# Optimization experiments

Measured on AMD Instinct MI355X. Metric: run time of the kernel, lower is better.

The kernel has to match this reference:

```python
import jax, jax.numpy as jnp
import numpy as np

N_NODES = 50000
N_EDGES = 800000
FEAT_IN = 128
POS_IN = 16
EDGE_FEAT_IN = 16
H = 64
L = 4


def _lin(k, fan_in, fan_out):
    kw, kb = jax.random.split(k)
    s = 1.0 / np.sqrt(fan_in)
    W = jax.random.uniform(kw, (fan_in, fan_out), minval=-s, maxval=s, dtype=jnp.float32)
    b = jax.random.uniform(kb, (fan_out,), minval=-s, maxval=s, dtype=jnp.float32)
    return W, b


def setup_inputs() -> dict:
    key = jax.random.key(0)
    ks = jax.random.split(key, 32)
    h = jax.random.normal(ks[0], (N_NODES, FEAT_IN), dtype=jnp.float32)
    e = jax.random.normal(ks[1], (N_EDGES, EDGE_FEAT_IN), dtype=jnp.float32)
    p = jax.random.normal(ks[2], (N_NODES, POS_IN), dtype=jnp.float32)
    edge_index = jax.random.randint(ks[3], (2, N_EDGES), 0, N_NODES, dtype=jnp.int64 if jax.config.x64_enabled else jnp.int32)
    he_W, he_b = _lin(ks[4], FEAT_IN, H)
    ee_W, ee_b = _lin(ks[5], EDGE_FEAT_IN, H)
    pe_W, pe_b = _lin(ks[6], POS_IN, H)

    def stack(fan_in, base):
        Ws, bs = [], []
        for i in range(L):
            W, b = _lin(jax.random.fold_in(ks[7], base * 100 + i), fan_in, H)
            Ws.append(W); bs.append(b)
        return jnp.stack(Ws), jnp.stack(bs)

    hm_W, hm_b = stack(5 * H, 0)  # h_message_mlp
    hu_W, hu_b = stack(2 * H, 1)  # h_update
    eu_W, eu_b = stack(3 * H, 2)  # e_update
    pm_W, pm_b = stack(3 * H, 3)  # p_message_mlp
    pu_W, pu_b = stack(2 * H, 4)  # p_update
    return dict(h=h, e=e, p=p, edge_index=edge_index,
                he_W=he_W, he_b=he_b, ee_W=ee_W, ee_b=ee_b, pe_W=pe_W, pe_b=pe_b,
                hm_W=hm_W, hm_b=hm_b, hu_W=hu_W, hu_b=hu_b,
                eu_W=eu_W, eu_b=eu_b, pm_W=pm_W, pm_b=pm_b, pu_W=pu_W, pu_b=pu_b)


def reference(h, e, p, edge_index, he_W, he_b, ee_W, ee_b, pe_W, pe_b,
              hm_W, hm_b, hu_W, hu_b, eu_W, eu_b, pm_W, pm_b, pu_W, pu_b):
    send, rec = edge_index[0], edge_index[1]
    n = h.shape[0]
    h = h @ he_W + he_b  # [N,H]
    e = e @ ee_W + ee_b  # [E,H]
    p = p @ pe_W + pe_b  # [N,H]
    for i in range(L):
        hp_send = jnp.concatenate((h[send], p[send]), axis=1)  # [E,2H]
        hp_rec = jnp.concatenate((h[rec], p[rec]), axis=1)     # [E,2H]
        h_msg = jnp.concatenate((hp_send, hp_rec, e), axis=1) @ hm_W[i] + hm_b[i]  # [E,H]
        h_agg = jax.ops.segment_sum(h_msg, rec, num_segments=n)  # [N,H]
        h = jnp.concatenate((h, h_agg), axis=1) @ hu_W[i] + hu_b[i]
        e = jnp.concatenate((h[send], h[rec], e), axis=1) @ eu_W[i] + eu_b[i]
        p_msg = jnp.concatenate((p[send], p[rec], e), axis=1) @ pm_W[i] + pm_b[i]
        p_agg = jax.ops.segment_sum(p_msg, rec, num_segments=n)
        p = jnp.concatenate((p, p_agg), axis=1) @ pu_W[i] + pu_b[i]
    return (h, p)
```

## Files before the change

kernel.cpp:

```cpp
#include <hip/hip_runtime.h>
#include <hip/hip_bf16.h>

#define NN 50000
#define NE 800000

typedef __hip_bfloat16 bf16;
typedef __attribute__((ext_vector_type(8))) short bf16x8s;
typedef __attribute__((ext_vector_type(4))) float f32x4;

#define OFF_HP     0L
#define OFF_HSUM   12800000L
#define OFF_PSUM   25600000L
#define OFF_ESUM   38400000L
#define OFF_EAGGA  41600000L
#define OFF_EAGGB  54400000L
#define OFF_WFMT   67200000L
#define OFF_ROWPTR 67716096L
#define OFF_COLIDX 67916100L
#define OFF_SSEND  71116100L
#define OFF_SEG    74316100L
#define OFF_CNT    77516100L
#define OFF_BSUM   77716100L

#define SCAN_B 196

#define FW_HE 0
#define FW_EE 8192
#define FW_PE 10240
#define FW_L0 12288
#define LSTR  61440
#define R_HAGG 0
#define R_HMR  12288
#define R_HU   20480
#define R_EUS  28672
#define R_EUR  32768
#define R_EUE  36864
#define R_PAGG 40960
#define R_PMR  49152
#define R_PU   53248

#define AGG_STRIDE 72

__device__ __forceinline__ bf16x8s bfrag(const bf16* w, int c, int t, int lane) {
    return *(const bf16x8s*)(w + ((long)(c*4 + t)*64 + lane)*8);
}
__device__ __forceinline__ bf16x8s cvt8(const float* fp) {
    float4 f0 = ((const float4*)fp)[0];
    float4 f1 = ((const float4*)fp)[1];
    bf16 tmp[8];
    tmp[0]=__float2bfloat16(f0.x); tmp[1]=__float2bfloat16(f0.y);
    tmp[2]=__float2bfloat16(f0.z); tmp[3]=__float2bfloat16(f0.w);
    tmp[4]=__float2bfloat16(f1.x); tmp[5]=__float2bfloat16(f1.y);
    tmp[6]=__float2bfloat16(f1.z); tmp[7]=__float2bfloat16(f1.w);
    return *(const bf16x8s*)tmp;
}

__global__ __launch_bounds__(256) void wfmt_k(
    const float* __restrict__ he, const float* __restrict__ ee, const float* __restrict__ pe,
    const float* __restrict__ hm, const float* __restrict__ hu, const float* __restrict__ eu,
    const float* __restrict__ pm, const float* __restrict__ pu, bf16* __restrict__ wf)
{
    int s = blockIdx.x;
    const float* src = nullptr; int rowoff = 0, Ksrc = 0, Kpad = 0, mode = 0, split = 0, gap = 0; long doff = 0;
    if      (s == 0) { src = he; Ksrc = 128; Kpad = 128; doff = FW_HE; }
    else if (s == 1) { src = ee; Ksrc = 16;  Kpad = 32;  doff = FW_EE; }
    else if (s == 2) { src = pe; Ksrc = 16;  Kpad = 32;  doff = FW_PE; }
    else {
        int i = (s - 3) / 9, g = (s - 3) % 9;
        long base = FW_L0 + (long)i*LSTR;
        const float* HM = hm + (long)i*320*64;
        const float* HU = hu + (long)i*128*64;
        const float* EU = eu + (long)i*192*64;
        const float* PM = pm + (long)i*192*64;
        const float* PU = pu + (long)i*128*64;
        switch (g) {
          case 0:  src=HM; mode=4; split=128; gap=128; Kpad=192; doff=base+R_HAGG; break;
          case 1:  src=HM; rowoff=128; Ksrc=128; Kpad=128; doff=base+R_HMR;  break;
          case 2:  src=HU; rowoff=0;   Ksrc=128; Kpad=128; doff=base+R_HU;   break;
          case 3:  src=EU; rowoff=0;   Ksrc=64;  Kpad=64;  doff=base+R_EUS;  break;
          case 4:  src=EU; rowoff=64;  Ksrc=64;  Kpad=64;  doff=base+R_EUR;  break;
          case 5:  src=EU; rowoff=128; Ksrc=64;  Kpad=64;  doff=base+R_EUE;  break;
          case 6:  src=PM; mode=4; split=64; gap=64; Kpad=128; doff=base+R_PAGG; break;
          case 7:  src=PM; rowoff=64;  Ksrc=64;  Kpad=64;  doff=base+R_PMR;  break;
          default: src=PU; rowoff=0;   Ksrc=128; Kpad=128; doff=base+R_PU;   break;
        }
    }
    int total = Kpad * 64;
    for (int idx = threadIdx.x; idx < total; idx += 256) {
        int j = idx & 7, l = (idx >> 3) & 63, ct = idx >> 9;
        int c = ct >> 2, t = ct & 3;
        int k = c*32 + (l >> 4)*8 + j;
        int n = t*16 + (l & 15);
        float v;
        if (mode == 4) v = src[(long)(k + (k >= split ? gap : 0))*64 + n];
        else           v = (k < Ksrc) ? src[(long)(rowoff + k)*64 + n] : 0.f;
        wf[doff + idx] = __float2bfloat16(v);
    }
}

__global__ __launch_bounds__(256) void hist_k(const int* __restrict__ rec, int* __restrict__ cnt)
{
    int e = blockIdx.x*256 + threadIdx.x;
    if (e < NE) atomicAdd(&cnt[rec[e]], 1);
}

__global__ __launch_bounds__(256) void scan1_k(const int* __restrict__ cnt, int* __restrict__ bsum)
{
    __shared__ int sdata[256];
    int tid = threadIdx.x;
    int i = blockIdx.x*256 + tid;
    sdata[tid] = (i < NN) ? cnt[i] : 0;
    __syncthreads();
    #pragma unroll
    for (int off = 128; off > 0; off >>= 1) {
        if (tid < off) sdata[tid] += sdata[tid + off];
        __syncthreads();
    }
    if (tid == 0) bsum[blockIdx.x] = sdata[0];
}

__global__ __launch_bounds__(256) void scan2_k(int* __restrict__ bsum)
{
    __shared__ int sdata[256];
    int tid = threadIdx.x;
    int v = (tid < SCAN_B) ? bsum[tid] : 0;
    sdata[tid] = v;
    __syncthreads();
    #pragma unroll
    for (int off = 1; off < 256; off <<= 1) {
        int t = (tid >= off) ? sdata[tid - off] : 0;
        __syncthreads();
        sdata[tid] += t;
        __syncthreads();
    }
    if (tid < SCAN_B) bsum[tid] = sdata[tid] - v;
}

__global__ __launch_bounds__(256) void scan3_k(const int* __restrict__ cnt,
    const int* __restrict__ bsum, int* __restrict__ rowptr)
{
    __shared__ int sdata[256];
    int tid = threadIdx.x;
    int i = blockIdx.x*256 + tid;
    sdata[tid] = (i < NN) ? cnt[i] : 0;
    __syncthreads();
    #pragma unroll
    for (int off = 1; off < 256; off <<= 1) {
        int t = (tid >= off) ? sdata[tid - off] : 0;
        __syncthreads();
        sdata[tid] += t;
        __syncthreads();
    }
    if (i < NN) rowptr[i + 1] = sdata[tid] + bsum[blockIdx.x];
    if (i == 0) rowptr[0] = 0;
}

__global__ __launch_bounds__(256) void scatter_k(const int* __restrict__ rec,
    const int* __restrict__ rowptr, int* __restrict__ cursor, int* __restrict__ colidx)
{
    int e = blockIdx.x*256 + threadIdx.x;
    if (e < NE) {
        int r = rec[e];
        int pos = atomicAdd(&cursor[r], 1);
        colidx[rowptr[r] + pos] = e;
    }
}

__global__ __launch_bounds__(256) void segfill_k(const int* __restrict__ rowptr, int* __restrict__ seg)
{
    int n = blockIdx.x*256 + threadIdx.x;
    if (n < NN) {
        int b = rowptr[n], e = rowptr[n + 1];
        for (int j = b; j < e; ++j) seg[j] = n;
    }
}

template <bool BOTH>
__global__ __launch_bounds__(256) void gsum64_k(const bf16* __restrict__ hp, int coff,
    const int* __restrict__ ssend, const int* __restrict__ seg,
    float* __restrict__ out1, float* __restrict__ out2)
{
    __shared__ int s_ids[256];
    __shared__ int s_seg[256];
    int tid = threadIdx.x, lane = tid & 63, wv = tid >> 6;
    int gbase = blockIdx.x*256;
    s_ids[tid] = ssend[gbase + tid];
    s_seg[tid] = seg[gbase + tid];
    __syncthreads();
    int j0 = wv*64;
    const bf16* base = hp + coff + lane;

    unsigned short va[16], vb[16], wa[16], wb[16];
    #pragma unroll
    for (int k = 0; k < 16; ++k) {
        long o = (long)s_ids[j0 + k]*128;
        va[k] = *(const unsigned short*)(base + o);
        if (BOTH) wa[k] = *(const unsigned short*)(base + o + 64);
    }

    float a = 0.f, b2 = 0.f;
    int cur = s_seg[j0];
    #pragma unroll
    for (int b = 0; b < 4; ++b) {
        if (b < 3) {
            #pragma unroll
            for (int k = 0; k < 16; ++k) {
                long o = (long)s_ids[j0 + (b+1)*16 + k]*128;
                vb[k] = *(const unsigned short*)(base + o);
                if (BOTH) wb[k] = *(const unsigned short*)(base + o + 64);
            }
        }
        #pragma unroll
        for (int k = 0; k < 16; ++k) {
            int n = s_seg[j0 + b*16 + k];
            if (n != cur) {
                atomicAdd(&out1[(long)cur*64 + lane], a);
                if (BOTH) atomicAdd(&out2[(long)cur*64 + lane], b2);
                a = 0.f; b2 = 0.f; cur = n;
            }
            a += __uint_as_float(((unsigned)va[k]) << 16);
            if (BOTH) b2 += __uint_as_float(((unsigned)wa[k]) << 16);
        }
        if (b < 3) {
            #pragma unroll
            for (int k = 0; k < 16; ++k) { va[k] = vb[k]; if (BOTH) wa[k] = wb[k]; }
        }
    }
    atomicAdd(&out1[(long)cur*64 + lane], a);
    if (BOTH) atomicAdd(&out2[(long)cur*64 + lane], b2);
}

__global__ __launch_bounds__(256) void esum_k(const float* __restrict__ e_in,
    const int* __restrict__ colidx, const int* __restrict__ seg, const int* __restrict__ send,
    int* __restrict__ ssend, float* __restrict__ esum)
{
    __shared__ int s_ids[256];
    __shared__ int s_seg[256];
    int tid = threadIdx.x;
    int gbase = blockIdx.x*256;
    int id = colidx[gbase + tid];
    s_ids[tid] = id;
    s_seg[tid] = seg[gbase + tid];
    ssend[gbase + tid] = send[id];
    __syncthreads();
    int grp = tid >> 4, c = tid & 15;
    int j0 = grp*16;
    float vv[16];
    #pragma unroll
    for (int jj = 0; jj < 16; ++jj) vv[jj] = e_in[(long)s_ids[j0 + jj]*16 + c];
    float a = 0.f;
    int cur = s_seg[j0];
    #pragma unroll
    for (int jj = 0; jj < 16; ++jj) {
        int n = s_seg[j0 + jj];
        if (n != cur) { atomicAdd(&esum[(long)cur*16 + c], a); a = 0.f; cur = n; }
        a += vv[jj];
    }
    atomicAdd(&esum[(long)cur*16 + c], a);
}

__global__ __launch_bounds__(256) void eembn_k(const float* __restrict__ esum,
    const int* __restrict__ deg, const bf16* __restrict__ wEE, const float* __restrict__ ee_b,
    float* __restrict__ eagg)
{
    int tid = threadIdx.x, lane = tid & 63, wv = tid >> 6;
    int l15 = lane & 15, q = lane >> 4;
    int row = blockIdx.x*64 + wv*16 + l15;
    int rc = (row < NN) ? row : NN - 1;
    f32x4 acc[4];
    #pragma unroll
    for (int t = 0; t < 4; ++t) { acc[t][0]=0; acc[t][1]=0; acc[t][2]=0; acc[t][3]=0; }
    {
        bf16x8s af = {0,0,0,0,0,0,0,0};
        if (q < 2) af = cvt8(esum + (long)rc*16 + q*8);
        #pragma unroll
        for (int t = 0; t < 4; ++t)
            acc[t] = __builtin_amdgcn_mfma_f32_16x16x32_bf16(af, bfrag(wEE, 0, t, lane), acc[t], 0, 0, 0);
    }
    float bv[4];
    #pragma unroll
    for (int t = 0; t < 4; ++t) bv[t] = ee_b[t*16 + l15];
    #pragma unroll
    for (int r = 0; r < 4; ++r) {
        int ro = blockIdx.x*64 + wv*16 + q*4 + r;
        if (ro < NN) {
            float dg = (float)deg[ro];
            #pragma unroll
            for (int t = 0; t < 4; ++t)
                eagg[(long)ro*64 + t*16 + l15] = acc[t][r] + dg*bv[t];
        }
    }
}

__global__ __launch_bounds__(256) void hemb_k(const float* __restrict__ h_in,
    const bf16* __restrict__ wHE, const float* __restrict__ he_b, bf16* __restrict__ hp)
{
    int tid = threadIdx.x, lane = tid & 63, wv = tid >> 6;
    int l15 = lane & 15, q = lane >> 4;
    int row = blockIdx.x*64 + wv*16 + l15;
    int rc = (row < NN) ? row : NN - 1;
    f32x4 acc[4];
    #pragma unroll
    for (int t = 0; t < 4; ++t) { float b = he_b[t*16 + l15]; acc[t][0]=b; acc[t][1]=b; acc[t][2]=b; acc[t][3]=b; }
    #pragma unroll
    for (int c = 0; c < 4; ++c) {
        bf16x8s af = cvt8(h_in + (long)rc*128 + c*32 + q*8);
        #pragma unroll
        for (int t = 0; t < 4; ++t)
            acc[t] = __builtin_amdgcn_mfma_f32_16x16x32_bf16(af, bfrag(wHE, c, t, lane), acc[t], 0, 0, 0);
    }
    #pragma unroll
    for (int r = 0; r < 4; ++r) {
        int ro = blockIdx.x*64 + wv*16 + q*4 + r;
        if (ro < NN)
            #pragma unroll
            for (int t = 0; t < 4; ++t) hp[(long)ro*128 + t*16 + l15] = __float2bfloat16(acc[t][r]);
    }
}

__global__ __launch_bounds__(256) void pemb_k(const float* __restrict__ p_in,
    const bf16* __restrict__ wPE, const float* __restrict__ pe_b, bf16* __restrict__ hp)
{
    int tid = threadIdx.x, lane = tid & 63, wv = tid >> 6;
    int l15 = lane & 15, q = lane >> 4;
    int row = blockIdx.x*64 + wv*16 + l15;
    int rc = (row < NN) ? row : NN - 1;
    f32x4 acc[4];
    #pragma unroll
    for (int t = 0; t < 4; ++t) { float b = pe_b[t*16 + l15]; acc[t][0]=b; acc[t][1]=b; acc[t][2]=b; acc[t][3]=b; }
    {
        bf16x8s af = {0,0,0,0,0,0,0,0};
        if (q < 2) af = cvt8(p_in + (long)rc*16 + q*8);
        #pragma unroll
        for (int t = 0; t < 4; ++t)
            acc[t] = __builtin_amdgcn_mfma_f32_16x16x32_bf16(af, bfrag(wPE, 0, t, lane), acc[t], 0, 0, 0);
    }
    #pragma unroll
    for (int r = 0; r < 4; ++r) {
        int ro = blockIdx.x*64 + wv*16 + q*4 + r;
        if (ro < NN)
            #pragma unroll
            for (int t = 0; t < 4; ++t) hp[(long)ro*128 + 64 + t*16 + l15] = __float2bfloat16(acc[t][r]);
    }
}

__global__ __launch_bounds__(256) void hfuse_k(
    bf16* __restrict__ hp, float* __restrict__ hsum, const float* __restrict__ psum,
    const float* __restrict__ eagg, const int* __restrict__ deg,
    const bf16* __restrict__ wAGG, const bf16* __restrict__ wR, const float* __restrict__ mb,
    const bf16* __restrict__ wU, const float* __restrict__ ub, float* __restrict__ out2)
{
    __shared__ __align__(16) bf16 sAgg[64 * AGG_STRIDE];
    int tid = threadIdx.x, lane = tid & 63, wv = tid >> 6;
    int l15 = lane & 15, q = lane >> 4;
    int row = blockIdx.x*64 + wv*16 + l15;
    int rc = (row < NN) ? row : NN - 1;

    f32x4 aA[4], aR[4];
    #pragma unroll
    for (int t = 0; t < 4; ++t) {
        aA[t][0]=0;aA[t][1]=0;aA[t][2]=0;aA[t][3]=0;
        aR[t][0]=0;aR[t][1]=0;aR[t][2]=0;aR[t][3]=0;
    }
    #pragma unroll
    for (int c = 0; c < 6; ++c) {
        bf16x8s af = (c < 2) ? cvt8(hsum + (long)rc*64 + c*32 + q*8)
                   : (c < 4) ? cvt8(psum + (long)rc*64 + (c-2)*32 + q*8)
                             : cvt8(eagg + (long)rc*64 + (c-4)*32 + q*8);
        #pragma unroll
        for (int t = 0; t < 4; ++t)
            aA[t] = __builtin_amdgcn_mfma_f32_16x16x32_bf16(af, bfrag(wAGG, c, t, lane), aA[t], 0, 0, 0);
    }
    if (row < NN) {
        float4 z4 = make_float4(0.f, 0.f, 0.f, 0.f);
        #pragma unroll
        for (int c = 0; c < 2; ++c) {
            *(float4*)(hsum + (long)rc*64 + c*32 + q*8)     = z4;
            *(float4*)(hsum + (long)rc*64 + c*32 + q*8 + 4) = z4;
        }
    }
    #pragma unroll
    for (int c = 0; c < 4; ++c) {
        bf16x8s af = *(const bf16x8s*)(hp + (long)rc*128 + c*32 + q*8);
        #pragma unroll
        for (int t = 0; t < 4; ++t)
            aR[t] = __builtin_amdgcn_mfma_f32_16x16x32_bf16(af, bfrag(wR, c, t, lane), aR[t], 0, 0, 0);
    }
    float mbv[4];
    #pragma unroll
    for (int t = 0; t < 4; ++t) mbv[t] = mb[t*16 + l15];
    #pragma unroll
    for (int r = 0; r < 4; ++r) {
        int ro = blockIdx.x*64 + wv*16 + q*4 + r;
        float dg = (float)deg[(ro < NN) ? ro : NN - 1];
        #pragma unroll
        for (int t = 0; t < 4; ++t)
            sAgg[(wv*16 + q*4 + r)*AGG_STRIDE + t*16 + l15] =
                __float2bfloat16(aA[t][r] + dg*(aR[t][r] + mbv[t]));
    }
    __syncthreads();
    f32x4 acc[4];
    #pragma unroll
    for (int t = 0; t < 4; ++t) { float b = ub[t*16 + l15]; acc[t][0]=b; acc[t][1]=b; acc[t][2]=b; acc[t][3]=b; }
    #pragma unroll
    for (int c = 0; c < 4; ++c) {
        bf16x8s af = (c < 2) ? *(const bf16x8s*)(hp + (long)rc*128 + c*32 + q*8)
                             : *(const bf16x8s*)(sAgg + (wv*16 + l15)*AGG_STRIDE + (c-2)*32 + q*8);
        #pragma unroll
        for (int t = 0; t < 4; ++t)
            acc[t] = __builtin_amdgcn_mfma_f32_16x16x32_bf16(af, bfrag(wU, c, t, lane), acc[t], 0, 0, 0);
    }
    #pragma unroll
    for (int r = 0; r < 4; ++r) {
        int ro = blockIdx.x*64 + wv*16 + q*4 + r;
        if (ro < NN) {
            #pragma unroll
            for (int t = 0; t < 4; ++t) {
                float fv = acc[t][r];
                hp[(long)ro*128 + t*16 + l15] = __float2bfloat16(fv);
                if (out2) out2[(long)ro*64 + t*16 + l15] = fv;
            }
        }
    }
}

__global__ __launch_bounds__(256) void pfuse_k(
    bf16* __restrict__ hp, const float* __restrict__ hsumN, float* __restrict__ psum,
    const float* __restrict__ eaggIn, float* __restrict__ eaggOut, const int* __restrict__ deg,
    const bf16* __restrict__ wEUS, const bf16* __restrict__ wEUR, const bf16* __restrict__ wEUE,
    const float* __restrict__ eub,
    const bf16* __restrict__ wAGG, const bf16* __restrict__ wR, const float* __restrict__ mb,
    const bf16* __restrict__ wU, const float* __restrict__ ub, float* __restrict__ out2)
{
    __shared__ __align__(16) bf16 sE[64 * AGG_STRIDE];
    __shared__ __align__(16) bf16 sAgg[64 * AGG_STRIDE];
    int tid = threadIdx.x, lane = tid & 63, wv = tid >> 6;
    int l15 = lane & 15, q = lane >> 4;
    int row = blockIdx.x*64 + wv*16 + l15;
    int rc = (row < NN) ? row : NN - 1;

    f32x4 aE[4], aH[4];
    #pragma unroll
    for (int t = 0; t < 4; ++t) {
        aE[t][0]=0;aE[t][1]=0;aE[t][2]=0;aE[t][3]=0;
        aH[t][0]=0;aH[t][1]=0;aH[t][2]=0;aH[t][3]=0;
    }
    #pragma unroll
    for (int c = 0; c < 4; ++c) {
        bf16x8s af = (c < 2) ? cvt8(hsumN + (long)rc*64 + c*32 + q*8)
                             : cvt8(eaggIn + (long)rc*64 + (c-2)*32 + q*8);
        #pragma unroll
        for (int t = 0; t < 4; ++t) {
            bf16x8s w = (c < 2) ? bfrag(wEUS, c, t, lane) : bfrag(wEUE, c-2, t, lane);
            aE[t] = __builtin_amdgcn_mfma_f32_16x16x32_bf16(af, w, aE[t], 0, 0, 0);
        }
    }
    #pragma unroll
    for (int c = 0; c < 2; ++c) {
        bf16x8s af = *(const bf16x8s*)(hp + (long)rc*128 + c*32 + q*8);
        #pragma unroll
        for (int t = 0; t < 4; ++t)
            aH[t] = __builtin_amdgcn_mfma_f32_16x16x32_bf16(af, bfrag(wEUR, c, t, lane), aH[t], 0, 0, 0);
    }
    float ebv[4];
    #pragma unroll
    for (int t = 0; t < 4; ++t) ebv[t] = eub[t*16 + l15];
    #pragma unroll
    for (int r = 0; r < 4; ++r) {
        int ro = blockIdx.x*64 + wv*16 + q*4 + r;
        float dg = (float)deg[(ro < NN) ? ro : NN - 1];
        #pragma unroll
        for (int t = 0; t < 4; ++t) {
            float ev = aE[t][r] + dg*(aH[t][r] + ebv[t]);
            sE[(wv*16 + q*4 + r)*AGG_STRIDE + t*16 + l15] = __float2bfloat16(ev);
            if (eaggOut && ro < NN) eaggOut[(long)ro*64 + t*16 + l15] = ev;
        }
    }
    __syncthreads();

    f32x4 aA[4], aR[4];
    #pragma unroll
    for (int t = 0; t < 4; ++t) {
        aA[t][0]=0;aA[t][1]=0;aA[t][2]=0;aA[t][3]=0;
        aR[t][0]=0;aR[t][1]=0;aR[t][2]=0;aR[t][3]=0;
    }
    #pragma unroll
    for (int c = 0; c < 4; ++c) {
        bf16x8s af = (c < 2) ? cvt8(psum + (long)rc*64 + c*32 + q*8)
                             : *(const bf16x8s*)(sE + (wv*16 + l15)*AGG_STRIDE + (c-2)*32 + q*8);
        #pragma unroll
        for (int t = 0; t < 4; ++t)
            aA[t] = __builtin_amdgcn_mfma_f32_16x16x32_bf16(af, bfrag(wAGG, c, t, lane), aA[t], 0, 0, 0);
    }
    if (row < NN) {
        float4 z4 = make_float4(0.f, 0.f, 0.f, 0.f);
        #pragma unroll
        for (int c = 0; c < 2; ++c) {
            *(float4*)(psum + (long)rc*64 + c*32 + q*8)     = z4;
            *(float4*)(psum + (long)rc*64 + c*32 + q*8 + 4) = z4;
        }
    }
    #pragma unroll
    for (int c = 0; c < 2; ++c) {
        bf16x8s af = *(const bf16x8s*)(hp + (long)rc*128 + 64 + c*32 + q*8);
        #pragma unroll
        for (int t = 0; t < 4; ++t)
            aR[t] = __builtin_amdgcn_mfma_f32_16x16x32_bf16(af, bfrag(wR, c, t, lane), aR[t], 0, 0, 0);
    }
    float mbv[4];
    #pragma unroll
    for (int t = 0; t < 4; ++t) mbv[t] = mb[t*16 + l15];
    #pragma unroll
    for (int r = 0; r < 4; ++r) {
        int ro = blockIdx.x*64 + wv*16 + q*4 + r;
        float dg = (float)deg[(ro < NN) ? ro : NN - 1];
        #pragma unroll
        for (int t = 0; t < 4; ++t)
            sAgg[(wv*16 + q*4 + r)*AGG_STRIDE + t*16 + l15] =
                __float2bfloat16(aA[t][r] + dg*(aR[t][r] + mbv[t]));
    }
    __syncthreads();
    f32x4 acc[4];
    #pragma unroll
    for (int t = 0; t < 4; ++t) { float b = ub[t*16 + l15]; acc[t][0]=b; acc[t][1]=b; acc[t][2]=b; acc[t][3]=b; }
    #pragma unroll
    for (int c = 0; c < 4; ++c) {
        bf16x8s af = (c < 2) ? *(const bf16x8s*)(hp + (long)rc*128 + 64 + c*32 + q*8)
                             : *(const bf16x8s*)(sAgg + (wv*16 + l15)*AGG_STRIDE + (c-2)*32 + q*8);
        #pragma unroll
        for (int t = 0; t < 4; ++t)
            acc[t] = __builtin_amdgcn_mfma_f32_16x16x32_bf16(af, bfrag(wU, c, t, lane), acc[t], 0, 0, 0);
    }
    #pragma unroll
    for (int r = 0; r < 4; ++r) {
        int ro = blockIdx.x*64 + wv*16 + q*4 + r;
        if (ro < NN) {
            #pragma unroll
            for (int t = 0; t < 4; ++t) {
                float fv = acc[t][r];
                hp[(long)ro*128 + 64 + t*16 + l15] = __float2bfloat16(fv);
                if (out2) out2[(long)ro*64 + t*16 + l15] = fv;
            }
        }
    }
}

extern "C" void kernel_launch(void* const* d_in, const int* in_sizes, int n_in,
                              void* d_out, int out_size, void* d_ws, size_t ws_size,
                              hipStream_t stream)
{
    (void)in_sizes; (void)n_in; (void)out_size; (void)ws_size;
    const float* h_in = (const float*)d_in[0];
    const float* e_in = (const float*)d_in[1];
    const float* p_in = (const float*)d_in[2];
    const int*  ei   = (const int*)d_in[3];
    const int* send = ei;
    const int* rec  = ei + NE;
    const float* he_W = (const float*)d_in[4];  const float* he_b = (const float*)d_in[5];
    const float* ee_W = (const float*)d_in[6];  const float* ee_b = (const float*)d_in[7];
    const float* pe_W = (const float*)d_in[8];  const float* pe_b = (const float*)d_in[9];
    const float* hm_W = (const float*)d_in[10]; const float* hm_b = (const float*)d_in[11];
    const float* hu_W = (const float*)d_in[12]; const float* hu_b = (const float*)d_in[13];
    const float* eu_W = (const float*)d_in[14]; const float* eu_b = (const float*)d_in[15];
    const float* pm_W = (const float*)d_in[16]; const float* pm_b = (const float*)d_in[17];
    const float* pu_W = (const float*)d_in[18]; const float* pu_b = (const float*)d_in[19];

    char* ws = (char*)d_ws;
    bf16* hp     = (bf16*)(ws + OFF_HP);
    float* hsum  = (float*)(ws + OFF_HSUM);
    float* psum  = (float*)(ws + OFF_PSUM);
    float* esum  = (float*)(ws + OFF_ESUM);
    float* eaggA = (float*)(ws + OFF_EAGGA);
    float* eaggB = (float*)(ws + OFF_EAGGB);
    bf16* wf     = (bf16*)(ws + OFF_WFMT);
    int* rowptr  = (int*)(ws + OFF_ROWPTR);
    int* colidx  = (int*)(ws + OFF_COLIDX);
    int* ssend   = (int*)(ws + OFF_SSEND);
    int* segarr  = (int*)(ws + OFF_SEG);
    int* cnt     = (int*)(ws + OFF_CNT);
    int* bsum    = (int*)(ws + OFF_BSUM);
    float* dout  = (float*)d_out;

    const int EB   = NE / 256;
    const int NB64 = (NN + 63) / 64;

    (void)hipMemsetAsync(cnt, 0, NN * sizeof(int), stream);
    hist_k<<<EB, 256, 0, stream>>>(rec, cnt);
    scan1_k<<<SCAN_B, 256, 0, stream>>>(cnt, bsum);
    scan2_k<<<1, 256, 0, stream>>>(bsum);
    scan3_k<<<SCAN_B, 256, 0, stream>>>(cnt, bsum, rowptr);
    (void)hipMemsetAsync(cnt, 0, NN * sizeof(int), stream);
    scatter_k<<<EB, 256, 0, stream>>>(rec, rowptr, cnt, colidx);
    segfill_k<<<SCAN_B, 256, 0, stream>>>(rowptr, segarr);

    (void)hipMemsetAsync(hsum, 0, (long)NN*(64 + 64 + 16)*sizeof(float), stream);

    esum_k<<<EB, 256, 0, stream>>>(e_in, colidx, segarr, send, ssend, esum);

    wfmt_k<<<39, 256, 0, stream>>>(he_W, ee_W, pe_W, hm_W, hu_W, eu_W, pm_W, pu_W, wf);

    hemb_k<<<NB64, 256, 0, stream>>>(h_in, wf + FW_HE, he_b, hp);
    pemb_k<<<NB64, 256, 0, stream>>>(p_in, wf + FW_PE, pe_b, hp);
    eembn_k<<<NB64, 256, 0, stream>>>(esum, cnt, wf + FW_EE, ee_b, eaggA);
    gsum64_k<true><<<EB, 256, 0, stream>>>(hp, 0, ssend, segarr, hsum, psum);

    float* eA = eaggA;
    float* eB = eaggB;
    for (int i = 0; i < 4; ++i) {
        long base = FW_L0 + (long)i*LSTR;
        hfuse_k<<<NB64, 256, 0, stream>>>(hp, hsum, psum, eA, cnt,
            wf + base + R_HAGG, wf + base + R_HMR, hm_b + i*64,
            wf + base + R_HU, hu_b + i*64,
            (i == 3) ? dout : nullptr);
        gsum64_k<false><<<EB, 256, 0, stream>>>(hp, 0, ssend, segarr, hsum, nullptr);
        pfuse_k<<<NB64, 256, 0, stream>>>(hp, hsum, psum, eA, (i < 3) ? eB : nullptr, cnt,
            wf + base + R_EUS, wf + base + R_EUR, wf + base + R_EUE, eu_b + i*64,
            wf + base + R_PAGG, wf + base + R_PMR, pm_b + i*64,
            wf + base + R_PU, pu_b + i*64,
            (i == 3) ? dout + (long)NN*64 : nullptr);
        if (i < 3)
            gsum64_k<false><<<EB, 256, 0, stream>>>(hp, 64, ssend, segarr, psum, nullptr);
        float* tmp = eA; eA = eB; eB = tmp;
    }
}
```

Baseline: 646.4 us.

## Store edge aggregates in bf16, fuse h/p embeddings, deepen gather prefetch

The per-node edge aggregate buffers change from fp32 to bf16, which halves their write and read traffic in eembn, hfuse and pfuse. The h and p embedding kernels become one launch that writes both halves of the hp row. The gather-sum kernel takes the prefetch depth as a template parameter and uses 32 loads in flight for the single-stream passes, trading extra registers for more memory-level parallelism. Keeping the edge aggregate in bf16 adds a rounding step that lowers its precision.

After: 657.3 us. About the same (+1.7%).

```diff
diff --git a/kernel.cpp b/kernel.cpp
--- a/kernel.cpp
+++ b/kernel.cpp
@@ -175,7 +175,7 @@
     }
 }
 
-template <bool BOTH>
+template <int DEPTH, bool BOTH>
 __global__ __launch_bounds__(256) void gsum64_k(const bf16* __restrict__ hp, int coff,
     const int* __restrict__ ssend, const int* __restrict__ seg,
     float* __restrict__ out1, float* __restrict__ out2)
@@ -189,10 +189,12 @@
     __syncthreads();
     int j0 = wv*64;
     const bf16* base = hp + coff + lane;
-
-    unsigned short va[16], vb[16], wa[16], wb[16];
-    #pragma unroll
-    for (int k = 0; k < 16; ++k) {
+    constexpr int NB = 64 / DEPTH;
+
+    unsigned short va[DEPTH], vb[DEPTH];
+    unsigned short wa[BOTH ? DEPTH : 1], wb[BOTH ? DEPTH : 1];
+    #pragma unroll
+    for (int k = 0; k < DEPTH; ++k) {
         long o = (long)s_ids[j0 + k]*128;
         va[k] = *(const unsigned short*)(base + o);
         if (BOTH) wa[k] = *(const unsigned short*)(base + o + 64);
@@ -201,18 +203,18 @@
     float a = 0.f, b2 = 0.f;
     int cur = s_seg[j0];
     #pragma unroll
-    for (int b = 0; b < 4; ++b) {
-        if (b < 3) {
+    for (int b = 0; b < NB; ++b) {
+        if (b < NB - 1) {
             #pragma unroll
-            for (int k = 0; k < 16; ++k) {
-                long o = (long)s_ids[j0 + (b+1)*16 + k]*128;
+            for (int k = 0; k < DEPTH; ++k) {
+                long o = (long)s_ids[j0 + (b+1)*DEPTH + k]*128;
                 vb[k] = *(const unsigned short*)(base + o);
                 if (BOTH) wb[k] = *(const unsigned short*)(base + o + 64);
             }
         }
         #pragma unroll
-        for (int k = 0; k < 16; ++k) {
-            int n = s_seg[j0 + b*16 + k];
+        for (int k = 0; k < DEPTH; ++k) {
+            int n = s_seg[j0 + b*DEPTH + k];
             if (n != cur) {
                 atomicAdd(&out1[(long)cur*64 + lane], a);
                 if (BOTH) atomicAdd(&out2[(long)cur*64 + lane], b2);
@@ -221,9 +223,9 @@
             a += __uint_as_float(((unsigned)va[k]) << 16);
             if (BOTH) b2 += __uint_as_float(((unsigned)wa[k]) << 16);
         }
-        if (b < 3) {
+        if (b < NB - 1) {
             #pragma unroll
-            for (int k = 0; k < 16; ++k) { va[k] = vb[k]; if (BOTH) wa[k] = wb[k]; }
+            for (int k = 0; k < DEPTH; ++k) { va[k] = vb[k]; if (BOTH) wa[k] = wb[k]; }
         }
     }
     atomicAdd(&out1[(long)cur*64 + lane], a);
@@ -261,7 +263,7 @@
 
 __global__ __launch_bounds__(256) void eembn_k(const float* __restrict__ esum,
     const int* __restrict__ deg, const bf16* __restrict__ wEE, const float* __restrict__ ee_b,
-    float* __restrict__ eagg)
+    bf16* __restrict__ eagg)
 {
     int tid = threadIdx.x, lane = tid & 63, wv = tid >> 6;
     int l15 = lane & 15, q = lane >> 4;
@@ -287,66 +289,56 @@
             float dg = (float)deg[ro];
             #pragma unroll
             for (int t = 0; t < 4; ++t)
-                eagg[(long)ro*64 + t*16 + l15] = acc[t][r] + dg*bv[t];
-        }
-    }
-}
-
-__global__ __launch_bounds__(256) void hemb_k(const float* __restrict__ h_in,
-    const bf16* __restrict__ wHE, const float* __restrict__ he_b, bf16* __restrict__ hp)
+                eagg[(long)ro*64 + t*16 + l15] = __float2bfloat16(acc[t][r] + dg*bv[t]);
+        }
+    }
+}
+
+__global__ __launch_bounds__(256) void hpemb_k(const float* __restrict__ h_in,
+    const float* __restrict__ p_in,
+    const bf16* __restrict__ wHE, const bf16* __restrict__ wPE,
+    const float* __restrict__ he_b, const float* __restrict__ pe_b, bf16* __restrict__ hp)
 {
     int tid = threadIdx.x, lane = tid & 63, wv = tid >> 6;
     int l15 = lane & 15, q = lane >> 4;
     int row = blockIdx.x*64 + wv*16 + l15;
     int rc = (row < NN) ? row : NN - 1;
-    f32x4 acc[4];
-    #pragma unroll
-    for (int t = 0; t < 4; ++t) { float b = he_b[t*16 + l15]; acc[t][0]=b; acc[t][1]=b; acc[t][2]=b; acc[t][3]=b; }
+    f32x4 aH[4], aP[4];
+    #pragma unroll
+    for (int t = 0; t < 4; ++t) {
+        float bh = he_b[t*16 + l15], bp = pe_b[t*16 + l15];
+        aH[t][0]=bh; aH[t][1]=bh; aH[t][2]=bh; aH[t][3]=bh;
+        aP[t][0]=bp; aP[t][1]=bp; aP[t][2]=bp; aP[t][3]=bp;
+    }
     #pragma unroll
     for (int c = 0; c < 4; ++c) {
         bf16x8s af = cvt8(h_in + (long)rc*128 + c*32 + q*8);
         #pragma unroll
         for (int t = 0; t < 4; ++t)
-            acc[t] = __builtin_amdgcn_mfma_f32_16x16x32_bf16(af, bfrag(wHE, c, t, lane), acc[t], 0, 0, 0);
+            aH[t] = __builtin_amdgcn_mfma_f32_16x16x32_bf16(af, bfrag(wHE, c, t, lane), aH[t], 0, 0, 0);
+    }
+    {
+        bf16x8s af = {0,0,0,0,0,0,0,0};
+        if (q < 2) af = cvt8(p_in + (long)rc*16 + q*8);
+        #pragma unroll
+        for (int t = 0; t < 4; ++t)
+            aP[t] = __builtin_amdgcn_mfma_f32_16x16x32_bf16(af, bfrag(wPE, 0, t, lane), aP[t], 0, 0, 0);
     }
     #pragma unroll
     for (int r = 0; r < 4; ++r) {
         int ro = blockIdx.x*64 + wv*16 + q*4 + r;
         if (ro < NN)
             #pragma unroll
-            for (int t = 0; t < 4; ++t) hp[(long)ro*128 + t*16 + l15] = __float2bfloat16(acc[t][r]);
-    }
-}
-
-__global__ __launch_bounds__(256) void pemb_k(const float* __restrict__ p_in,
-    const bf16* __restrict__ wPE, const float* __restrict__ pe_b, bf16* __restrict__ hp)
-{
-    int tid = threadIdx.x, lane = tid & 63, wv = tid >> 6;
-    int l15 = lane & 15, q = lane >> 4;
-    int row = blockIdx.x*64 + wv*16 + l15;
-    int rc = (row < NN) ? row : NN - 1;
-    f32x4 acc[4];
-    #pragma unroll
-    for (int t = 0; t < 4; ++t) { float b = pe_b[t*16 + l15]; acc[t][0]=b; acc[t][1]=b; acc[t][2]=b; acc[t][3]=b; }
-    {
-        bf16x8s af = {0,0,0,0,0,0,0,0};
-        if (q < 2) af = cvt8(p_in + (long)rc*16 + q*8);
-        #pragma unroll
-        for (int t = 0; t < 4; ++t)
-            acc[t] = __builtin_amdgcn_mfma_f32_16x16x32_bf16(af, bfrag(wPE, 0, t, lane), acc[t], 0, 0, 0);
-    }
-    #pragma unroll
-    for (int r = 0; r < 4; ++r) {
-        int ro = blockIdx.x*64 + wv*16 + q*4 + r;
-        if (ro < NN)
-            #pragma unroll
-            for (int t = 0; t < 4; ++t) hp[(long)ro*128 + 64 + t*16 + l15] = __float2bfloat16(acc[t][r]);
+            for (int t = 0; t < 4; ++t) {
+                hp[(long)ro*128 + t*16 + l15]      = __float2bfloat16(aH[t][r]);
+                hp[(long)ro*128 + 64 + t*16 + l15] = __float2bfloat16(aP[t][r]);
+            }
     }
 }
 
 __global__ __launch_bounds__(256) void hfuse_k(
     bf16* __restrict__ hp, float* __restrict__ hsum, const float* __restrict__ psum,
-    const float* __restrict__ eagg, const int* __restrict__ deg,
+    const bf16* __restrict__ eagg, const int* __restrict__ deg,
     const bf16* __restrict__ wAGG, const bf16* __restrict__ wR, const float* __restrict__ mb,
     const bf16* __restrict__ wU, const float* __restrict__ ub, float* __restrict__ out2)
 {
@@ -366,7 +358,7 @@
     for (int c = 0; c < 6; ++c) {
         bf16x8s af = (c < 2) ? cvt8(hsum + (long)rc*64 + c*32 + q*8)
                    : (c < 4) ? cvt8(psum + (long)rc*64 + (c-2)*32 + q*8)
-                             : cvt8(eagg + (long)rc*64 + (c-4)*32 + q*8);
+                             : *(const bf16x8s*)(eagg + (long)rc*64 + (c-4)*32 + q*8);
         #pragma unroll
         for (int t = 0; t < 4; ++t)
             aA[t] = __builtin_amdgcn_mfma_f32_16x16x32_bf16(af, bfrag(wAGG, c, t, lane), aA[t], 0, 0, 0);
@@ -426,7 +418,7 @@
 
 __global__ __launch_bounds__(256) void pfuse_k(
     bf16* __restrict__ hp, const float* __restrict__ hsumN, float* __restrict__ psum,
-    const float* __restrict__ eaggIn, float* __restrict__ eaggOut, const int* __restrict__ deg,
+    const bf16* __restrict__ eaggIn, bf16* __restrict__ eaggOut, const int* __restrict__ deg,
     const bf16* __restrict__ wEUS, const bf16* __restrict__ wEUR, const bf16* __restrict__ wEUE,
     const float* __restrict__ eub,
     const bf16* __restrict__ wAGG, const bf16* __restrict__ wR, const float* __restrict__ mb,
@@ -448,7 +440,7 @@
     #pragma unroll
     for (int c = 0; c < 4; ++c) {
         bf16x8s af = (c < 2) ? cvt8(hsumN + (long)rc*64 + c*32 + q*8)
-                             : cvt8(eaggIn + (long)rc*64 + (c-2)*32 + q*8);
+                             : *(const bf16x8s*)(eaggIn + (long)rc*64 + (c-2)*32 + q*8);
         #pragma unroll
         for (int t = 0; t < 4; ++t) {
             bf16x8s w = (c < 2) ? bfrag(wEUS, c, t, lane) : bfrag(wEUE, c-2, t, lane);
@@ -471,8 +463,8 @@
         float dg = (float)deg[(ro < NN) ? ro : NN - 1];
         #pragma unroll
         for (int t = 0; t < 4; ++t) {
-            float ev = aE[t][r] + dg*(aH[t][r] + ebv[t]);
-            sE[(wv*16 + q*4 + r)*AGG_STRIDE + t*16 + l15] = __float2bfloat16(ev);
+            bf16 ev = __float2bfloat16(aE[t][r] + dg*(aH[t][r] + ebv[t]));
+            sE[(wv*16 + q*4 + r)*AGG_STRIDE + t*16 + l15] = ev;
             if (eaggOut && ro < NN) eaggOut[(long)ro*64 + t*16 + l15] = ev;
         }
     }
@@ -570,8 +562,8 @@
     float* hsum  = (float*)(ws + OFF_HSUM);
     float* psum  = (float*)(ws + OFF_PSUM);
     float* esum  = (float*)(ws + OFF_ESUM);
-    float* eaggA = (float*)(ws + OFF_EAGGA);
-    float* eaggB = (float*)(ws + OFF_EAGGB);
+    bf16* eaggA  = (bf16*)(ws + OFF_EAGGA);
+    bf16* eaggB  = (bf16*)(ws + OFF_EAGGB);
     bf16* wf     = (bf16*)(ws + OFF_WFMT);
     int* rowptr  = (int*)(ws + OFF_ROWPTR);
     int* colidx  = (int*)(ws + OFF_COLIDX);
@@ -599,27 +591,26 @@
 
     wfmt_k<<<39, 256, 0, stream>>>(he_W, ee_W, pe_W, hm_W, hu_W, eu_W, pm_W, pu_W, wf);
 
-    hemb_k<<<NB64, 256, 0, stream>>>(h_in, wf + FW_HE, he_b, hp);
-    pemb_k<<<NB64, 256, 0, stream>>>(p_in, wf + FW_PE, pe_b, hp);
+    hpemb_k<<<NB64, 256, 0, stream>>>(h_in, p_in, wf + FW_HE, wf + FW_PE, he_b, pe_b, hp);
     eembn_k<<<NB64, 256, 0, stream>>>(esum, cnt, wf + FW_EE, ee_b, eaggA);
-    gsum64_k<true><<<EB, 256, 0, stream>>>(hp, 0, ssend, segarr, hsum, psum);
-
-    float* eA = eaggA;
-    float* eB = eaggB;
+    gsum64_k<16, true><<<EB, 256, 0, stream>>>(hp, 0, ssend, segarr, hsum, psum);
+
+    bf16* eA = eaggA;
+    bf16* eB = eaggB;
     for (int i = 0; i < 4; ++i) {
         long base = FW_L0 + (long)i*LSTR;
         hfuse_k<<<NB64, 256, 0, stream>>>(hp, hsum, psum, eA, cnt,
             wf + base + R_HAGG, wf + base + R_HMR, hm_b + i*64,
             wf + base + R_HU, hu_b + i*64,
             (i == 3) ? dout : nullptr);
-        gsum64_k<false><<<EB, 256, 0, stream>>>(hp, 0, ssend, segarr, hsum, nullptr);
+        gsum64_k<32, false><<<EB, 256, 0, stream>>>(hp, 0, ssend, segarr, hsum, nullptr);
         pfuse_k<<<NB64, 256, 0, stream>>>(hp, hsum, psum, eA, (i < 3) ? eB : nullptr, cnt,
             wf + base + R_EUS, wf + base + R_EUR, wf + base + R_EUE, eu_b + i*64,
             wf + base + R_PAGG, wf + base + R_PMR, pm_b + i*64,
             wf + base + R_PU, pu_b + i*64,
             (i == 3) ? dout + (long)NN*64 : nullptr);
         if (i < 3)
-            gsum64_k<false><<<EB, 256, 0, stream>>>(hp, 64, ssend, segarr, psum, nullptr);
-        float* tmp = eA; eA = eB; eB = tmp;
-    }
-}
+            gsum64_k<32, false><<<EB, 256, 0, stream>>>(hp, 64, ssend, segarr, psum, nullptr);
+        bf16* tmp = eA; eA = eB; eB = tmp;
+    }
+}
```
